# Kernel tuning notes

Hardware: AMD Instinct MI355X
Metric: run time of the kernel (lower is better)

The kernel has to match this reference:

```python
import jax, jax.numpy as jnp
import numpy as np

S, B, T = 2048, 256, 48


def setup_inputs() -> dict:
    key = jax.random.key(0)
    k1, k2, k3, k4 = jax.random.split(key, 4)
    emissions = jax.random.normal(k1, (S, B, T), dtype=jnp.float32)
    tags = jax.random.randint(k2, (S, B), 0, T, dtype=jnp.int64)
    mask = jnp.ones((S, B), dtype=jnp.int32)
    # params initialized uniform(-0.1, 0.1) as in reset_parameters
    start_transitions = jax.random.uniform(k3, (T,), minval=-0.1, maxval=0.1, dtype=jnp.float32)
    end_transitions = jax.random.uniform(k4, (T,), minval=-0.1, maxval=0.1, dtype=jnp.float32)
    transitions = jax.random.uniform(jax.random.fold_in(key, 7), (T, T), minval=-0.1, maxval=0.1, dtype=jnp.float32)
    return {
        "emissions": emissions,
        "tags": tags,
        "mask": mask,
        "start_transitions": start_transitions,
        "end_transitions": end_transitions,
        "transitions": transitions,
    }


def _compute_score(emissions, tags, mask, start_transitions, end_transitions, transitions):
    # emissions: (S,B,T), tags/mask: (S,B)
    seq_length, batch_size = tags.shape
    maskf = mask.astype(emissions.dtype)
    ar = jnp.arange(batch_size)
    # emission score of the chosen tag at every step: (S,B)
    em_scores = jnp.take_along_axis(emissions, tags[..., None], axis=2)[..., 0]
    score = start_transitions[tags[0]] + em_scores[0]
    # transition scores between consecutive tags, masked: (S-1,B)
    trans_scores = transitions[tags[:-1], tags[1:]] * maskf[1:]
    score = score + trans_scores.sum(axis=0) + (em_scores[1:] * maskf[1:]).sum(axis=0)
    seq_ends = mask.astype(jnp.int32).sum(axis=0) - 1  # (B,)
    last_tags = tags[seq_ends, ar]
    score = score + end_transitions[last_tags]
    return score  # (B,)


def _compute_normalizer(emissions, mask, start_transitions, end_transitions, transitions):
    # forward algorithm via lax.scan over time
    score0 = start_transitions + emissions[0]  # (B,T)

    def step(score, inp):
        em_i, m_i = inp  # (B,T), (B,)
        # (B, T_prev, T_next)
        next_score = jax.nn.logsumexp(score[:, :, None] + transitions[None, :, :] + em_i[:, None, :], axis=1)
        score = jnp.where(m_i[:, None] != 0, next_score, score)
        return score, None

    score, _ = jax.lax.scan(step, score0, (emissions[1:], mask[1:]))
    score = score + end_transitions
    return jax.nn.logsumexp(score, axis=1)  # (B,)


def reference(emissions, tags, mask, start_transitions, end_transitions, transitions):
    numerator = _compute_score(emissions, tags, mask, start_transitions, end_transitions, transitions)
    denominator = _compute_normalizer(emissions, mask, start_transitions, end_transitions, transitions)
    llh = numerator - denominator
    return llh.sum()  # reduction='sum'
```

## Files before the change

### kernel.cpp

```cpp
#include <hip/hip_runtime.h>
#include <hip/hip_bf16.h>
#include <math.h>

#define S_LEN  2048
#define B_SZ   256
#define T_TAGS 48
#define MAT_U32 1152

#define WS_CNT_OFF 0
#define WS_K_OFF   1024
#define WS_P_OFF   65536

using short8 = __attribute__((ext_vector_type(8))) short;
using f32x4  = __attribute__((ext_vector_type(4))) float;
using f32x2  = __attribute__((ext_vector_type(2))) float;

#if defined(__has_builtin) && __has_builtin(__builtin_amdgcn_exp2f)
#define EXP2N(x) __builtin_amdgcn_exp2f(x)
#else
#define EXP2N(x) __expf((x) * 0.6931471805599453f)
#endif

__device__ __forceinline__ unsigned cvtpk(float lo, float hi) {
    unsigned r;
    asm("v_cvt_pk_bf16_f32 %0, %1, %2" : "=v"(r) : "v"(lo), "v"(hi));
    return r;
}
__device__ __forceinline__ unsigned pk2bf(float lo, float hi) {
    __hip_bfloat162 h2 = __float22bfloat162_rn(make_float2(lo, hi));
    return *reinterpret_cast<unsigned*>(&h2);
}

template<int CCH>
__global__ __launch_bounds__(64, 4) void crf_chunk_kernel(
    const float* __restrict__ em, const int* __restrict__ mask,
    const float* __restrict__ trans, unsigned* __restrict__ wsP,
    int* __restrict__ wsK, int* __restrict__ wsCnt)
{
    constexpr int LCH = S_LEN / CCH;
    constexpr int NQ  = (LCH + 63) / 64;
    const int bid = blockIdx.x;
    const int b = bid / CCH, c = bid % CCH;
    const int tid = threadIdx.x;
    const int cc = tid & 15, g = tid >> 4;
    const int start = c * LCH;

    __shared__ __align__(16) uint4 lds4[320];
    char* Lc = (char*)lds4;

#pragma unroll
    for (int i = 0; i < 5; ++i) lds4[tid + 64 * i] = make_uint4(0u, 0u, 0u, 0u);
    __builtin_amdgcn_wave_barrier();
    if (tid < T_TAGS)
        *(unsigned short*)(Lc + (tid >> 4) * 1536 +
                           ((tid >> 3) * 16 + (tid & 15)) * 16 + (tid & 7) * 2) = 0x3F80;
    __builtin_amdgcn_wave_barrier();

    unsigned long long ball[NQ];
    int cnt = 0;
#pragma unroll
    for (int q = 0; q < NQ; ++q) {
        const int s = start + q * 64 + tid;
        ball[q] = __ballot(mask[s * B_SZ + b] != 0);
        cnt += (int)__popcll(ball[q]);
    }
    if (tid == 0) atomicAdd(&wsCnt[b], cnt);
    if (c == 0) ball[0] &= ~1ull;

    short8 Afr[3][2];
#pragma unroll
    for (int jt = 0; jt < 3; ++jt) {
        const int j = jt * 16 + cc;
#pragma unroll
        for (int kt = 0; kt < 2; ++kt) {
            unsigned u[4];
#pragma unroll
            for (int h = 0; h < 4; ++h) {
                const int ka = kt * 16 + 8 * g + 2 * h;
                const float lo = (kt == 0 || ka >= 32) ? __expf(trans[ka * T_TAGS + j]) : 0.f;
                const float hi = (kt == 0 || ka + 1 >= 32) ? __expf(trans[(ka + 1) * T_TAGS + j]) : 0.f;
                u[h] = cvtpk(lo, hi);
            }
            uint4 uu = make_uint4(u[0], u[1], u[2], u[3]);
            Afr[jt][kt] = *reinterpret_cast<short8*>(&uu);
        }
    }

    int K = 0, pend = 0;
    float kf = 0.0f;
    const f32x4 fz = {0.f, 0.f, 0.f, 0.f};
    const size_t embase = (size_t)b * T_TAGS + 4 * g;

    auto emload = [&](int t, f32x4& d0, f32x4& d1, f32x4& d2) {
        int ss = start + t; if (ss > S_LEN - 1) ss = S_LEN - 1;
        const float* p = em + (size_t)ss * (B_SZ * T_TAGS) + embase;
        d0 = *(const f32x4*)(p);
        d1 = *(const f32x4*)(p + 16);
        d2 = *(const f32x4*)(p + 32);
    };

    auto step = [&](bool on, bool probe,
                    const f32x4& e0, const f32x4& e1, const f32x4& e2) {
        if (!on) return;
        const short8 B00 = *(const short8*)(Lc +               tid * 16);
        const short8 B01 = *(const short8*)(Lc +         512 + tid * 16);
        const short8 B10 = *(const short8*)(Lc + 1536 +        tid * 16);
        const short8 B11 = *(const short8*)(Lc + 1536 + 512 + tid * 16);
        const short8 B20 = *(const short8*)(Lc + 3072 +        tid * 16);
        const short8 B21 = *(const short8*)(Lc + 3072 + 512 + tid * 16);
        constexpr float L2E = 1.4426950408889634f;
        const float kf_ = kf;
        kf = 0.0f;
        pend = 0;
        const f32x2 kf2 = {kf_, kf_};
        const f32x2 l2e2 = {L2E, L2E};
        f32x2 x0a = (f32x2){e0[0], e0[1]} * l2e2 + kf2;
        f32x2 x0b = (f32x2){e0[2], e0[3]} * l2e2 + kf2;
        f32x2 x1a = (f32x2){e1[0], e1[1]} * l2e2 + kf2;
        f32x2 x1b = (f32x2){e1[2], e1[3]} * l2e2 + kf2;
        f32x2 x2a = (f32x2){e2[0], e2[1]} * l2e2 + kf2;
        f32x2 x2b = (f32x2){e2[2], e2[3]} * l2e2 + kf2;
        const f32x2 ef0a = {EXP2N(x0a[0]), EXP2N(x0a[1])};
        const f32x2 ef0b = {EXP2N(x0b[0]), EXP2N(x0b[1])};
        const f32x2 ef1a = {EXP2N(x1a[0]), EXP2N(x1a[1])};
        const f32x2 ef1b = {EXP2N(x1b[0]), EXP2N(x1b[1])};
        const f32x2 ef2a = {EXP2N(x2a[0]), EXP2N(x2a[1])};
        const f32x2 ef2b = {EXP2N(x2b[0]), EXP2N(x2b[1])};
        f32x4 z;
#define DOFRAG(JT, NT, BN0, BN1, EFa, EFb, PROBE_)                             \
        z = __builtin_amdgcn_mfma_f32_16x16x32_bf16(Afr[JT][0], BN0, fz, 0, 0, 0); \
        z = __builtin_amdgcn_mfma_f32_16x16x32_bf16(Afr[JT][1], BN1, z,  0, 0, 0); \
        if (PROBE_) {                                                          \
            const unsigned pb_ = (unsigned)__builtin_amdgcn_readfirstlane(     \
                (int)__float_as_uint(z[0]));                                   \
            const int ee_ = (int)((pb_ >> 23) & 255u);                         \
            const int kk_ = ee_ - 127;                                         \
            K += kk_; pend = kk_;                                              \
            kf = (float)(-kk_);                                                \
        }                                                                      \
        {                                                                      \
            const f32x2 zl_ = (f32x2){z[0], z[1]} * (EFa);                     \
            const f32x2 zh_ = (f32x2){z[2], z[3]} * (EFb);                     \
            *(uint2*)(Lc + (NT) * 1536 +                                       \
                      ((2 * (JT) + (g >> 1)) * 16 + cc) * 16 + (g & 1) * 8) =  \
                make_uint2(cvtpk(zl_[0], zl_[1]), cvtpk(zh_[0], zh_[1]));      \
        }

        DOFRAG(0, 0, B00, B01, ef0a, ef0b, probe);
        DOFRAG(0, 1, B10, B11, ef0a, ef0b, false);
        DOFRAG(0, 2, B20, B21, ef0a, ef0b, false);
        DOFRAG(1, 0, B00, B01, ef1a, ef1b, false);
        DOFRAG(1, 1, B10, B11, ef1a, ef1b, false);
        DOFRAG(1, 2, B20, B21, ef1a, ef1b, false);
        DOFRAG(2, 0, B00, B01, ef2a, ef2b, false);
        DOFRAG(2, 1, B10, B11, ef2a, ef2b, false);
        DOFRAG(2, 2, B20, B21, ef2a, ef2b, false);
#undef DOFRAG
    };

    f32x4 a0, a1, a2, b0, b1, b2;
    emload(0, a0, a1, a2);
    emload(1, b0, b1, b2);

#pragma unroll
    for (int q = 0; q < NQ; ++q) {
        const unsigned long long bq = ball[q];
        for (int tt = 0; tt < 64; tt += 2) {
            const int t = q * 64 + tt;
            step(((bq >> tt) & 1ull) != 0, (tt & 3) == 0, a0, a1, a2);
            emload(t + 2, a0, a1, a2);
            step(((bq >> (tt + 1)) & 1ull) != 0, false, b0, b1, b2);
            emload(t + 3, b0, b1, b2);
        }
    }

    auto mkI = [&](int shift) -> short8 {
        const int e = cc + shift - 8 * g;
        uint4 uu;
        uu.x = (e == 0) ? 0x3F80u : (e == 1) ? 0x3F800000u : 0u;
        uu.y = (e == 2) ? 0x3F80u : (e == 3) ? 0x3F800000u : 0u;
        uu.z = (e == 4) ? 0x3F80u : (e == 5) ? 0x3F800000u : 0u;
        uu.w = (e == 6) ? 0x3F80u : (e == 7) ? 0x3F800000u : 0u;
        return *reinterpret_cast<short8*>(&uu);
    };
    const short8 I0  = mkI(0);
    const short8 I16 = mkI(16);

    short8 F0[3], F1[3];
#pragma unroll
    for (int nt = 0; nt < 3; ++nt) {
        F0[nt] = *(const short8*)(Lc + nt * 1536 +       tid * 16);
        F1[nt] = *(const short8*)(Lc + nt * 1536 + 512 + tid * 16);
    }
#pragma unroll
    for (int nt = 0; nt < 3; ++nt) {
#pragma unroll
        for (int ct = 0; ct < 3; ++ct) {
            const short8 Af = (ct < 2) ? F0[nt] : F1[nt];
            const short8 Bi = (ct == 0) ? I0 : I16;
            f32x4 z = __builtin_amdgcn_mfma_f32_16x16x32_bf16(Af, Bi, fz, 0, 0, 0);
            const int jcol = ct * 16 + cc;
            *(uint2*)&wsP[(size_t)bid * MAT_U32 + jcol * 24 + nt * 8 + g * 2] =
                make_uint2(pk2bf(z[0], z[1]), pk2bf(z[2], z[3]));
        }
    }
    if (tid == 0) wsK[bid] = K - pend;
}

template<int CCH>
__global__ __launch_bounds__(64, 1) void crf_combine_kernel(
    const float* __restrict__ em, const int* __restrict__ mask,
    const float* __restrict__ startT, const float* __restrict__ endT,
    const float* __restrict__ trans, const unsigned* __restrict__ wsP,
    const int* __restrict__ wsK, const int* __restrict__ wsCnt,
    const int* __restrict__ tags, float* __restrict__ out)
{
    const int b = blockIdx.x, tid = threadIdx.x;
    const int j = (tid < T_TAGS) ? tid : 0;

    float nacc = 0.f;
#pragma unroll 4
    for (int q = 0; q < S_LEN / 64; ++q) {
        const int s = q * 64 + tid;
        if (s == 0) {
            const int t0 = tags[b];
            nacc += em[(size_t)b * T_TAGS + t0] + startT[t0];
        } else if (mask[s * B_SZ + b] != 0) {
            const int tc = tags[(size_t)s * B_SZ + b];
            const int tp = tags[(size_t)(s - 1) * B_SZ + b];
            nacc += em[((size_t)s * B_SZ + b) * T_TAGS + tc] + trans[tp * T_TAGS + tc];
        }
    }
#pragma unroll
    for (int off = 32; off > 0; off >>= 1) nacc += __shfl_down(nacc, off);

    float v = (tid < T_TAGS) ? __expf(startT[j] + em[(size_t)b * T_TAGS + j]) : 0.f;
    int K2 = 0;
    for (int c = 0; c < CCH; ++c) {
        const unsigned base = (unsigned)(b * CCH + c) * MAT_U32 + j * 24;
        uint4 W[6];
#pragma unroll
        for (int q = 0; q < 6; ++q)
            W[q] = *reinterpret_cast<const uint4*>(&wsP[base + 4 * q]);
        float a0 = 0.f, a1 = 0.f;
#pragma unroll
        for (int q = 0; q < 6; ++q) {
            const unsigned wv[4] = {W[q].x, W[q].y, W[q].z, W[q].w};
#pragma unroll
            for (int r = 0; r < 4; ++r) {
                const int i = q * 8 + r * 2;
                const float p0 = __uint_as_float(wv[r] << 16);
                const float p1 = __uint_as_float(wv[r] & 0xFFFF0000u);
                a0 = fmaf(__uint_as_float(__builtin_amdgcn_readlane(__float_as_uint(v), i)), p0, a0);
                a1 = fmaf(__uint_as_float(__builtin_amdgcn_readlane(__float_as_uint(v), i + 1)), p1, a1);
            }
        }
        const float vn = a0 + a1;
        const unsigned pb = (unsigned)__builtin_amdgcn_readfirstlane((int)__float_as_uint(vn));
        const int ee = (int)((pb >> 23) & 255u);
        const float sc = __uint_as_float((unsigned)(254 - ee) << 23);
        v = vn * sc;
        K2 += (ee - 127) + wsK[b * CCH + c];
    }
    float contrib = (tid < T_TAGS) ? v * __expf(endT[j]) : 0.f;
#pragma unroll
    for (int off = 32; off > 0; off >>= 1) contrib += __shfl_down(contrib, off);
    if (tid == 0) {
        const int cnt  = wsCnt[b];
        const int last = tags[(size_t)(cnt - 1) * B_SZ + b];
        const double den = (double)K2 * 0.6931471805599453 + (double)__logf(contrib);
        atomicAdd(out, nacc + endT[last] + (float)(-den));
    }
}

extern "C" void kernel_launch(void* const* d_in, const int* in_sizes, int n_in,
                              void* d_out, int out_size, void* d_ws, size_t ws_size,
                              hipStream_t stream)
{
    const float* em     = (const float*)d_in[0];
    const int*   tags   = (const int*)  d_in[1];
    const int*   mask   = (const int*)  d_in[2];
    const float* startT = (const float*)d_in[3];
    const float* endT   = (const float*)d_in[4];
    const float* trans  = (const float*)d_in[5];
    float* out = (float*)d_out;

    int*      wsCnt = (int*)((char*)d_ws + WS_CNT_OFF);
    int*      wsK   = (int*)((char*)d_ws + WS_K_OFF);
    unsigned* wsP   = (unsigned*)((char*)d_ws + WS_P_OFF);

    hipMemsetAsync(out, 0, sizeof(float), stream);
    hipMemsetAsync(wsCnt, 0, B_SZ * sizeof(int), stream);

    const size_t need32 = (size_t)WS_P_OFF + (size_t)(B_SZ * 32) * (MAT_U32 * 4);
    const size_t need16 = (size_t)WS_P_OFF + (size_t)(B_SZ * 16) * (MAT_U32 * 4);
    if (ws_size >= need32) {
        crf_chunk_kernel<32><<<B_SZ * 32, 64, 0, stream>>>(em, mask, trans, wsP, wsK, wsCnt);
        crf_combine_kernel<32><<<B_SZ, 64, 0, stream>>>(em, mask, startT, endT, trans, wsP, wsK, wsCnt, tags, out);
    } else if (ws_size >= need16) {
        crf_chunk_kernel<16><<<B_SZ * 16, 64, 0, stream>>>(em, mask, trans, wsP, wsK, wsCnt);
        crf_combine_kernel<16><<<B_SZ, 64, 0, stream>>>(em, mask, startT, endT, trans, wsP, wsK, wsCnt, tags, out);
    } else {
        crf_chunk_kernel<8><<<B_SZ * 8, 64, 0, stream>>>(em, mask, trans, wsP, wsK, wsCnt);
        crf_combine_kernel<8><<<B_SZ, 64, 0, stream>>>(em, mask, startT, endT, trans, wsP, wsK, wsCnt, tags, out);
    }
}
```

Measured before the change: 232.5 us.

## Drop 32-chunk path, move mask count into 4-wave combine kernel

Measured after the change: 197.2 us. -15.2%, faster.

```diff
diff --git a/kernel.cpp b/kernel.cpp
--- a/kernel.cpp
+++ b/kernel.cpp
@@ -7,7 +7,6 @@
 #define T_TAGS 48
 #define MAT_U32 1152
 
-#define WS_CNT_OFF 0
 #define WS_K_OFF   1024
 #define WS_P_OFF   65536
 
@@ -35,7 +34,7 @@
 __global__ __launch_bounds__(64, 4) void crf_chunk_kernel(
     const float* __restrict__ em, const int* __restrict__ mask,
     const float* __restrict__ trans, unsigned* __restrict__ wsP,
-    int* __restrict__ wsK, int* __restrict__ wsCnt)
+    int* __restrict__ wsK)
 {
     constexpr int LCH = S_LEN / CCH;
     constexpr int NQ  = (LCH + 63) / 64;
@@ -45,11 +44,11 @@
     const int cc = tid & 15, g = tid >> 4;
     const int start = c * LCH;
 
-    __shared__ __align__(16) uint4 lds4[320];
+    __shared__ __align__(16) uint4 lds4[288];
     char* Lc = (char*)lds4;
 
 #pragma unroll
-    for (int i = 0; i < 5; ++i) lds4[tid + 64 * i] = make_uint4(0u, 0u, 0u, 0u);
+    for (int i = 0; i < 5; ++i) { const int idx = tid + 64 * i; if (idx < 288) lds4[idx] = make_uint4(0u, 0u, 0u, 0u); }
     __builtin_amdgcn_wave_barrier();
     if (tid < T_TAGS)
         *(unsigned short*)(Lc + (tid >> 4) * 1536 +
@@ -57,14 +56,11 @@
     __builtin_amdgcn_wave_barrier();
 
     unsigned long long ball[NQ];
-    int cnt = 0;
 #pragma unroll
     for (int q = 0; q < NQ; ++q) {
         const int s = start + q * 64 + tid;
         ball[q] = __ballot(mask[s * B_SZ + b] != 0);
-        cnt += (int)__popcll(ball[q]);
-    }
-    if (tid == 0) atomicAdd(&wsCnt[b], cnt);
+    }
     if (c == 0) ball[0] &= ~1ull;
 
     short8 Afr[3][2];
@@ -208,33 +204,48 @@
 }
 
 template<int CCH>
-__global__ __launch_bounds__(64, 1) void crf_combine_kernel(
+__global__ __launch_bounds__(256, 1) void crf_combine_kernel(
     const float* __restrict__ em, const int* __restrict__ mask,
     const float* __restrict__ startT, const float* __restrict__ endT,
     const float* __restrict__ trans, const unsigned* __restrict__ wsP,
-    const int* __restrict__ wsK, const int* __restrict__ wsCnt,
-    const int* __restrict__ tags, float* __restrict__ out)
+    const int* __restrict__ wsK, const int* __restrict__ tags,
+    float* __restrict__ out)
 {
     const int b = blockIdx.x, tid = threadIdx.x;
-    const int j = (tid < T_TAGS) ? tid : 0;
+    const int lane = tid & 63, wid = tid >> 6;
+
+    __shared__ float s_nacc[4];
+    __shared__ int   s_cnt[4];
 
     float nacc = 0.f;
-#pragma unroll 4
-    for (int q = 0; q < S_LEN / 64; ++q) {
-        const int s = q * 64 + tid;
+    int cnt = 0;
+    for (int q = wid; q < S_LEN / 64; q += 4) {
+        const int s = q * 64 + lane;
+        const int mk = mask[s * B_SZ + b];
+        cnt += (mk != 0);
         if (s == 0) {
             const int t0 = tags[b];
             nacc += em[(size_t)b * T_TAGS + t0] + startT[t0];
-        } else if (mask[s * B_SZ + b] != 0) {
+        } else if (mk != 0) {
             const int tc = tags[(size_t)s * B_SZ + b];
             const int tp = tags[(size_t)(s - 1) * B_SZ + b];
             nacc += em[((size_t)s * B_SZ + b) * T_TAGS + tc] + trans[tp * T_TAGS + tc];
         }
     }
 #pragma unroll
-    for (int off = 32; off > 0; off >>= 1) nacc += __shfl_down(nacc, off);
-
-    float v = (tid < T_TAGS) ? __expf(startT[j] + em[(size_t)b * T_TAGS + j]) : 0.f;
+    for (int off = 32; off > 0; off >>= 1) {
+        nacc += __shfl_down(nacc, off);
+        cnt  += __shfl_down(cnt, off);
+    }
+    if (lane == 0) { s_nacc[wid] = nacc; s_cnt[wid] = cnt; }
+    __syncthreads();
+    if (tid >= 64) return;
+
+    const float nall = s_nacc[0] + s_nacc[1] + s_nacc[2] + s_nacc[3];
+    const int   call = s_cnt[0] + s_cnt[1] + s_cnt[2] + s_cnt[3];
+
+    const int j = (lane < T_TAGS) ? lane : 0;
+    float v = (lane < T_TAGS) ? __expf(startT[j] + em[(size_t)b * T_TAGS + j]) : 0.f;
     int K2 = 0;
     for (int c = 0; c < CCH; ++c) {
         const unsigned base = (unsigned)(b * CCH + c) * MAT_U32 + j * 24;
@@ -262,14 +273,13 @@
         v = vn * sc;
         K2 += (ee - 127) + wsK[b * CCH + c];
     }
-    float contrib = (tid < T_TAGS) ? v * __expf(endT[j]) : 0.f;
+    float contrib = (lane < T_TAGS) ? v * __expf(endT[j]) : 0.f;
 #pragma unroll
     for (int off = 32; off > 0; off >>= 1) contrib += __shfl_down(contrib, off);
-    if (tid == 0) {
-        const int cnt  = wsCnt[b];
-        const int last = tags[(size_t)(cnt - 1) * B_SZ + b];
+    if (lane == 0) {
+        const int last = tags[(size_t)(call - 1) * B_SZ + b];
         const double den = (double)K2 * 0.6931471805599453 + (double)__logf(contrib);
-        atomicAdd(out, nacc + endT[last] + (float)(-den));
+        atomicAdd(out, nall + endT[last] + (float)(-den));
     }
 }
 
@@ -285,23 +295,17 @@
     const float* trans  = (const float*)d_in[5];
     float* out = (float*)d_out;
 
-    int*      wsCnt = (int*)((char*)d_ws + WS_CNT_OFF);
-    int*      wsK   = (int*)((char*)d_ws + WS_K_OFF);
-    unsigned* wsP   = (unsigned*)((char*)d_ws + WS_P_OFF);
+    int*      wsK = (int*)((char*)d_ws + WS_K_OFF);
+    unsigned* wsP = (unsigned*)((char*)d_ws + WS_P_OFF);
 
     hipMemsetAsync(out, 0, sizeof(float), stream);
-    hipMemsetAsync(wsCnt, 0, B_SZ * sizeof(int), stream);
-
-    const size_t need32 = (size_t)WS_P_OFF + (size_t)(B_SZ * 32) * (MAT_U32 * 4);
+
     const size_t need16 = (size_t)WS_P_OFF + (size_t)(B_SZ * 16) * (MAT_U32 * 4);
-    if (ws_size >= need32) {
-        crf_chunk_kernel<32><<<B_SZ * 32, 64, 0, stream>>>(em, mask, trans, wsP, wsK, wsCnt);
-        crf_combine_kernel<32><<<B_SZ, 64, 0, stream>>>(em, mask, startT, endT, trans, wsP, wsK, wsCnt, tags, out);
-    } else if (ws_size >= need16) {
-        crf_chunk_kernel<16><<<B_SZ * 16, 64, 0, stream>>>(em, mask, trans, wsP, wsK, wsCnt);
-        crf_combine_kernel<16><<<B_SZ, 64, 0, stream>>>(em, mask, startT, endT, trans, wsP, wsK, wsCnt, tags, out);
+    if (ws_size >= need16) {
+        crf_chunk_kernel<16><<<B_SZ * 16, 64, 0, stream>>>(em, mask, trans, wsP, wsK);
+        crf_combine_kernel<16><<<B_SZ, 256, 0, stream>>>(em, mask, startT, endT, trans, wsP, wsK, tags, out);
     } else {
-        crf_chunk_kernel<8><<<B_SZ * 8, 64, 0, stream>>>(em, mask, trans, wsP, wsK, wsCnt);
-        crf_combine_kernel<8><<<B_SZ, 64, 0, stream>>>(em, mask, startT, endT, trans, wsP, wsK, wsCnt, tags, out);
-    }
-}
+        crf_chunk_kernel<8><<<B_SZ * 8, 64, 0, stream>>>(em, mask, trans, wsP, wsK);
+        crf_combine_kernel<8><<<B_SZ, 256, 0, stream>>>(em, mask, startT, endT, trans, wsP, wsK, tags, out);
+    }
+}
```
